# Kernel tuning notes

Measured on AMD Instinct MI355X. Metric: run time of the kernel, lower is better.

The kernel has to match this reference:

```python
import jax, jax.numpy as jnp
import numpy as np

D_MODEL = 1024
NUM_HEADS = 16
HEAD_DIM = D_MODEL // NUM_HEADS


def setup_inputs() -> dict:
    key = jax.random.key(0)
    k_x, k_qkv, k_o = jax.random.split(key, 3)
    B, L = 2, 2048
    x = jax.random.normal(k_x, (B, L, D_MODEL), dtype=jnp.float32)
    # torch Linear weight [out, in]; y = x @ W.T. Scale ~ kaiming-uniform-ish.
    s = 1.0 / np.sqrt(D_MODEL)
    W_qkv = jax.random.uniform(k_qkv, (3 * D_MODEL, D_MODEL), dtype=jnp.float32, minval=-s, maxval=s)
    W_o = jax.random.uniform(k_o, (D_MODEL, D_MODEL), dtype=jnp.float32, minval=-s, maxval=s)
    return {"x": x, "W_qkv": W_qkv, "W_o": W_o}


def reference(x, W_qkv, W_o):
    B, L, D = x.shape
    H, dk = NUM_HEADS, HEAD_DIM
    qkv = (x @ W_qkv.T).reshape(B, L, 3, H, dk)
    q = qkv[:, :, 0].transpose(0, 2, 1, 3)  # [B,H,L,dk]
    k = qkv[:, :, 1].transpose(0, 2, 1, 3)
    v = qkv[:, :, 2].transpose(0, 2, 1, 3)
    scale = 1.0 / np.sqrt(dk).astype(np.float32)
    attn = jnp.einsum('bhqd,bhkd->bhqk', q, k) * scale  # [B,H,L,L]
    causal = jnp.tril(jnp.ones((L, L), dtype=bool))
    attn = jnp.where(causal, attn, -jnp.inf)
    attn = jax.nn.softmax(attn, axis=-1)
    y = jnp.einsum('bhqk,bhkd->bhqd', attn, v)  # [B,H,L,dk]
    y = y.transpose(0, 2, 1, 3).reshape(B, L, D)
    return y @ W_o.T
```

## Files before the change

kernel.cpp:

```cpp
#include <hip/hip_runtime.h>

typedef unsigned short u16;
typedef unsigned int   u32;

typedef __attribute__((ext_vector_type(4))) float  f32x4;
typedef __attribute__((ext_vector_type(8))) __bf16 bf16x8;

#define B_  2
#define L_  2048
#define H_  16

__device__ static inline u16 f2bf(float f) {
  u32 u = __builtin_bit_cast(u32, f);
  u32 r = u + 0x7fffu + ((u >> 16) & 1u);
  return (u16)(r >> 16);
}
__device__ static inline u32 pack2(float a, float b) {
  return (u32)f2bf(a) | ((u32)f2bf(b) << 16);
}
__device__ static inline u32 pack2t(float a, float b) {
  return __builtin_amdgcn_perm(__builtin_bit_cast(u32, b),
                               __builtin_bit_cast(u32, a), 0x07060302u);
}

__device__ static inline void gload_lds16(const u16* g, u16* lds) {
  __builtin_amdgcn_global_load_lds((__attribute__((address_space(1))) void*)(g),
                                   (__attribute__((address_space(3))) void*)(lds),
                                   16, 0, 0);
}

__global__ __launch_bounds__(256) void cvt3_kernel(
    const float4* __restrict__ a, uint2* __restrict__ ao, int na,
    const float4* __restrict__ b, uint2* __restrict__ bo, int nb,
    const float4* __restrict__ c, uint2* __restrict__ co, int nc)
{
  const int step = gridDim.x * 256;
  constexpr int nq = 1024 * 1024 / 4;
  for (int i = blockIdx.x * 256 + threadIdx.x; i < na; i += step) {
    float4 f = a[i];
    ao[i] = make_uint2(pack2(f.x, f.y), pack2(f.z, f.w));
  }
  for (int i = blockIdx.x * 256 + threadIdx.x; i < nb; i += step) {
    float4 f = b[i];
    const float s = (i < nq) ? 0.125f : 1.0f;
    bo[i] = make_uint2(pack2(f.x * s, f.y * s), pack2(f.z * s, f.w * s));
  }
  for (int i = blockIdx.x * 256 + threadIdx.x; i < nc; i += step) {
    float4 f = c[i];
    co[i] = make_uint2(pack2(f.x, f.y), pack2(f.z, f.w));
  }
}

template <bool OUT_F32, int NT, bool DBUF>
__global__ __launch_bounds__(256) void gemm_bt_kernel(
    const u16* __restrict__ A, const u16* __restrict__ Bt, void* __restrict__ Cv,
    const int K, const int N)
{
  constexpr int NB = DBUF ? 2 : 1;
  constexpr int JT = NT / 32;
  __shared__ __attribute__((aligned(16))) u16 Al[NB][128 * 64];
  __shared__ __attribute__((aligned(16))) u16 Bl[NB][NT * 64];

  const int tid  = threadIdx.x;
  const int w    = tid >> 6;
  const int lane = tid & 63;
  const int m0 = blockIdx.y * 128;
  const int n0 = blockIdx.x * NT;
  const int mo = (w >> 1) * 64;
  const int no = (w & 1) * (NT / 2);

  const int sr8  = lane >> 3;
  const int scol = (((lane & 7) ^ ((lane >> 3) & 7)) * 8);

  const f32x4 zero = {0.f, 0.f, 0.f, 0.f};
  f32x4 acc[4][JT];
  #pragma unroll
  for (int i = 0; i < 4; ++i)
    #pragma unroll
    for (int j = 0; j < JT; ++j) acc[i][j] = zero;

  const int frow = lane & 15;
  const int fg   = lane >> 4;

  auto stage = [&](int buf, int k0) {
    #pragma unroll
    for (int inst = 0; inst < 4; ++inst) {
      const int r = w * 32 + inst * 8 + sr8;
      gload_lds16(A + (size_t)(m0 + r) * K + k0 + scol, &Al[buf][(w * 32 + inst * 8) * 64]);
    }
    #pragma unroll
    for (int inst = 0; inst < NT / 32; ++inst) {
      const int r = w * (NT / 4) + inst * 8 + sr8;
      gload_lds16(Bt + (size_t)(n0 + r) * K + k0 + scol, &Bl[buf][(w * (NT / 4) + inst * 8) * 64]);
    }
  };

  if (DBUF) stage(0, 0);

  int cur = 0;
  for (int k0 = 0; k0 < K; k0 += 64) {
    __syncthreads();
    if (DBUF) {
      if (k0 + 64 < K) stage(cur ^ 1, k0 + 64);
    } else {
      stage(0, k0);
      __syncthreads();
    }
    #pragma unroll
    for (int ks = 0; ks < 2; ++ks) {
      const int fco = ((ks * 4 + fg) ^ (frow & 7)) * 8;
      bf16x8 af[4], bfr[JT];
      #pragma unroll
      for (int i = 0; i < 4; ++i)
        af[i] = *(const bf16x8*)&Al[cur][(mo + i * 16 + frow) * 64 + fco];
      #pragma unroll
      for (int j = 0; j < JT; ++j)
        bfr[j] = *(const bf16x8*)&Bl[cur][(no + j * 16 + frow) * 64 + fco];
      #pragma unroll
      for (int i = 0; i < 4; ++i)
        #pragma unroll
        for (int j = 0; j < JT; ++j)
          acc[i][j] = __builtin_amdgcn_mfma_f32_16x16x32_bf16(af[i], bfr[j], acc[i][j], 0, 0, 0);
    }
    if (DBUF) cur ^= 1;
  }

  const int crow0 = m0 + mo + (lane >> 4) * 4;
  const int ccol0 = n0 + no + (lane & 15);
  #pragma unroll
  for (int i = 0; i < 4; ++i)
    #pragma unroll
    for (int j = 0; j < JT; ++j)
      #pragma unroll
      for (int r = 0; r < 4; ++r) {
        const size_t idx = (size_t)(crow0 + i * 16 + r) * N + (ccol0 + j * 16);
        if (OUT_F32) ((float*)Cv)[idx] = acc[i][j][r];
        else         ((u16*)Cv)[idx]   = f2bf(acc[i][j][r]);
      }
}

__global__ __launch_bounds__(256) void attn_mfma_kernel(const u16* __restrict__ qkv,
                                                        u16* __restrict__ y)
{
  __shared__ __attribute__((aligned(16))) unsigned char smem[40960];

  const int tid  = threadIdx.x;
  const int w    = tid >> 6;
  const int lane = tid & 63;
  const int fr   = lane & 15;
  const int fg   = lane >> 4;
  const int bh   = blockIdx.x;
  const int bb   = bh >> 4;
  const int hh   = bh & 15;
  const size_t rb = (size_t)bb * L_;

  const int a  = blockIdx.y & 7;
  const int cc = blockIdx.y >> 3;
  const int qt = (cc == 0) ? a : (cc == 1) ? (31 - a) : (cc == 2) ? (8 + a) : (23 - a);

  u16* Kt  = (u16*)(smem);
  u32* Vtd = (u32*)(smem + 16384);
  u32* PTd = (u32*)(smem + 32768) + w * 512;

  const int kkp = lane & 31;
  const int dc  = 2 * w + (lane >> 5);

  const int ksr = w * 16 + (lane >> 3);
  const int ksc = (((lane & 7) ^ ((lane >> 3) & 7)) * 8);
  const int kco0 = ((fg) ^ (fr & 7)) * 8;
  const int kco1 = ((4 + fg) ^ (fr & 7)) * 8;

  const int cro0 = 4 * ((fg) ^ (fr & 7));
  const int cro1 = 4 * ((4 + fg) ^ (fr & 7));
  const int pwo  = 4 * (fr & 7);

  const f32x4 zero = {0.f, 0.f, 0.f, 0.f};

  const int q0 = qt * 64;
  const int qw = q0 + w * 16;
  const int n  = qt + 1;

  const bf16x8 qf0 = *(const bf16x8*)(qkv + (rb + qw + fr) * 3072 + hh * 64 + fg * 8);
  const bf16x8 qf1 = *(const bf16x8*)(qkv + (rb + qw + fr) * 3072 + hh * 64 + 32 + fg * 8);

  f32x4 oacc[4];
  #pragma unroll
  for (int mt = 0; mt < 4; ++mt) oacc[mt] = zero;
  float lsum = 0.f;

  {
    #pragma unroll
    for (int inst = 0; inst < 2; ++inst)
      gload_lds16(qkv + (rb + ksr + inst * 8) * 3072 + 1024 + hh * 64 + ksc,
                  &Kt[(w * 16 + inst * 8) * 64]);
    const u16* vp = qkv + (rb + 2 * kkp) * 3072 + 2048 + hh * 64 + dc * 8;
    uint4 va = *(const uint4*)vp;
    uint4 vb = *(const uint4*)(vp + 3072);
    u16 a16[8], b16[8];
    *(uint4*)a16 = va; *(uint4*)b16 = vb;
    #pragma unroll
    for (int i = 0; i < 8; ++i)
      Vtd[(dc * 8 + i) * 32 + 4 * ((kkp >> 2) ^ i) + (kkp & 3)] =
          (u32)a16[i] | ((u32)b16[i] << 16);
  }

  int cur = 0;
  for (int it = 0; it < n; ++it) {
    __syncthreads();

    const int  kt       = it * 64;
    const bool havenext = (it + 1) < n;
    uint4 va, vb;
    if (havenext) {
      #pragma unroll
      for (int inst = 0; inst < 2; ++inst)
        gload_lds16(qkv + (rb + kt + 64 + ksr + inst * 8) * 3072 + 1024 + hh * 64 + ksc,
                    &Kt[(cur ^ 1) * 4096 + (w * 16 + inst * 8) * 64]);
      const u16* vp = qkv + (rb + kt + 64 + 2 * kkp) * 3072 + 2048 + hh * 64 + dc * 8;
      va = *(const uint4*)vp;
      vb = *(const uint4*)(vp + 3072);
    }

    f32x4 sacc[4];
    #pragma unroll
    for (int nt = 0; nt < 4; ++nt) sacc[nt] = zero;
    __builtin_amdgcn_s_setprio(1);
    #pragma unroll
    for (int nt = 0; nt < 4; ++nt) {
      bf16x8 kf0 = *(const bf16x8*)&Kt[cur * 4096 + (nt * 16 + fr) * 64 + kco0];
      sacc[nt] = __builtin_amdgcn_mfma_f32_16x16x32_bf16(kf0, qf0, sacc[nt], 0, 0, 0);
      bf16x8 kf1 = *(const bf16x8*)&Kt[cur * 4096 + (nt * 16 + fr) * 64 + kco1];
      sacc[nt] = __builtin_amdgcn_mfma_f32_16x16x32_bf16(kf1, qf1, sacc[nt], 0, 0, 0);
    }
    __builtin_amdgcn_s_setprio(0);

    if (kt == q0) {
      #pragma unroll
      for (int nt = 0; nt < 4; ++nt) {
        float p[4];
        #pragma unroll
        for (int r = 0; r < 4; ++r) {
          p[r] = (nt * 16 + 4 * fg + r > w * 16 + fr) ? 0.f : __expf(sacc[nt][r]);
          lsum += p[r];
        }
        *(uint2*)&PTd[fr * 32 + ((8 * nt + 2 * fg) ^ pwo)] =
            make_uint2(pack2t(p[0], p[1]), pack2t(p[2], p[3]));
      }
    } else {
      #pragma unroll
      for (int nt = 0; nt < 4; ++nt) {
        float p[4];
        #pragma unroll
        for (int r = 0; r < 4; ++r) {
          p[r] = __expf(sacc[nt][r]);
          lsum += p[r];
        }
        *(uint2*)&PTd[fr * 32 + ((8 * nt + 2 * fg) ^ pwo)] =
            make_uint2(pack2t(p[0], p[1]), pack2t(p[2], p[3]));
      }
    }

    __builtin_amdgcn_s_setprio(1);
    #pragma unroll
    for (int ks = 0; ks < 2; ++ks) {
      bf16x8 pf = *(const bf16x8*)&PTd[fr * 32 + (ks ? cro1 : cro0)];
      #pragma unroll
      for (int mt = 0; mt < 4; ++mt) {
        bf16x8 vf = *(const bf16x8*)&Vtd[cur * 2048 + (mt * 16 + fr) * 32 + (ks ? cro1 : cro0)];
        oacc[mt] = __builtin_amdgcn_mfma_f32_16x16x32_bf16(vf, pf, oacc[mt], 0, 0, 0);
      }
    }
    __builtin_amdgcn_s_setprio(0);

    if (havenext) {
      u16 a16[8], b16[8];
      *(uint4*)a16 = va; *(uint4*)b16 = vb;
      #pragma unroll
      for (int i = 0; i < 8; ++i)
        Vtd[(cur ^ 1) * 2048 + (dc * 8 + i) * 32 + 4 * ((kkp >> 2) ^ i) + (kkp & 3)] =
            (u32)a16[i] | ((u32)b16[i] << 16);
    }
    cur ^= 1;
  }

  lsum += __shfl_xor(lsum, 16);
  lsum += __shfl_xor(lsum, 32);
  const float inv = 1.f / lsum;

  u16* yp = y + (rb + qw + fr) * 1024 + hh * 64 + 4 * fg;
  #pragma unroll
  for (int mt = 0; mt < 4; ++mt) {
    f32x4 o = oacc[mt];
    *(uint2*)(yp + mt * 16) = make_uint2(pack2(o[0] * inv, o[1] * inv),
                                         pack2(o[2] * inv, o[3] * inv));
  }
}

extern "C" void kernel_launch(void* const* d_in, const int* in_sizes, int n_in,
                              void* d_out, int out_size, void* d_ws, size_t ws_size,
                              hipStream_t stream)
{
  const float* x    = (const float*)d_in[0];
  const float* Wqkv = (const float*)d_in[1];
  const float* Wo   = (const float*)d_in[2];
  float* out = (float*)d_out;

  u16* xb    = (u16*)d_ws;
  u16* Wqkvb = xb    + (size_t)4096 * 1024;
  u16* Wob   = Wqkvb + (size_t)3072 * 1024;
  u16* qkv   = Wob   + (size_t)1024 * 1024;
  u16* y     = qkv   + (size_t)4096 * 3072;

  cvt3_kernel<<<dim3(2048), dim3(256), 0, stream>>>(
      (const float4*)x,    (uint2*)xb,    4096 * 1024 / 4,
      (const float4*)Wqkv, (uint2*)Wqkvb, 3072 * 1024 / 4,
      (const float4*)Wo,   (uint2*)Wob,   1024 * 1024 / 4);

  gemm_bt_kernel<false, 128, false><<<dim3(3072 / 128, 4096 / 128), dim3(256), 0, stream>>>(
      xb, Wqkvb, qkv, 1024, 3072);
  attn_mfma_kernel<<<dim3(B_ * H_, 32), dim3(256), 0, stream>>>(qkv, y);
  gemm_bt_kernel<true, 64, true><<<dim3(1024 / 64, 4096 / 128), dim3(256), 0, stream>>>(
      y, Wob, out, 1024, 1024);
}
```

Before: 169.3 us.

## Use two waves per attention block with 32 query rows each and register-permuted P

The attention kernel now runs 128 threads per block, and each wave handles 32 query rows instead of 16, so every K and V fragment read from LDS feeds two MFMAs. The P tile no longer goes through an LDS round trip. It is rearranged in registers with permlane32/permlane16 swaps, which removes the PTd buffer and shrinks LDS to 32 KB. Each thread now stages more K and V per iteration. The change raises register pressure and halves the threads per block, which may reduce latency hiding.

```diff
diff --git a/kernel.cpp b/kernel.cpp
--- a/kernel.cpp
+++ b/kernel.cpp
@@ -4,6 +4,7 @@
 typedef unsigned int   u32;
 
 typedef __attribute__((ext_vector_type(4))) float  f32x4;
+typedef __attribute__((ext_vector_type(4))) u32    u32x4;
 typedef __attribute__((ext_vector_type(8))) __bf16 bf16x8;
 
 #define B_  2
@@ -21,6 +22,15 @@
 __device__ static inline u32 pack2t(float a, float b) {
   return __builtin_amdgcn_perm(__builtin_bit_cast(u32, b),
                                __builtin_bit_cast(u32, a), 0x07060302u);
+}
+
+__device__ static inline void swap32p(u32& a, u32& b) {
+  auto r = __builtin_amdgcn_permlane32_swap(a, b, false, false);
+  a = r[0]; b = r[1];
+}
+__device__ static inline void swap16p(u32& a, u32& b) {
+  auto r = __builtin_amdgcn_permlane16_swap(a, b, false, false);
+  a = r[0]; b = r[1];
 }
 
 __device__ static inline void gload_lds16(const u16* g, u16* lds) {
@@ -139,10 +149,10 @@
       }
 }
 
-__global__ __launch_bounds__(256) void attn_mfma_kernel(const u16* __restrict__ qkv,
+__global__ __launch_bounds__(128) void attn_mfma_kernel(const u16* __restrict__ qkv,
                                                         u16* __restrict__ y)
 {
-  __shared__ __attribute__((aligned(16))) unsigned char smem[40960];
+  __shared__ __attribute__((aligned(16))) unsigned char smem[32768];
 
   const int tid  = threadIdx.x;
   const int w    = tid >> 6;
@@ -160,48 +170,65 @@
 
   u16* Kt  = (u16*)(smem);
   u32* Vtd = (u32*)(smem + 16384);
-  u32* PTd = (u32*)(smem + 32768) + w * 512;
-
-  const int kkp = lane & 31;
-  const int dc  = 2 * w + (lane >> 5);
-
-  const int ksr = w * 16 + (lane >> 3);
-  const int ksc = (((lane & 7) ^ ((lane >> 3) & 7)) * 8);
+
+  const int kkp = tid & 31;
+  const int dc  = tid >> 5;
+
+  const int ksr  = lane >> 3;
+  const int ksc  = (((lane & 7) ^ ((lane >> 3) & 7)) * 8);
   const int kco0 = ((fg) ^ (fr & 7)) * 8;
   const int kco1 = ((4 + fg) ^ (fr & 7)) * 8;
-
   const int cro0 = 4 * ((fg) ^ (fr & 7));
   const int cro1 = 4 * ((4 + fg) ^ (fr & 7));
-  const int pwo  = 4 * (fr & 7);
+
+  const int q0 = qt * 64;
+  const int qw = q0 + w * 32;
+  const int n  = qt + 1;
+
+  const bf16x8 qf00 = *(const bf16x8*)(qkv + (rb + qw + fr) * 3072 + hh * 64 + fg * 8);
+  const bf16x8 qf01 = *(const bf16x8*)(qkv + (rb + qw + fr) * 3072 + hh * 64 + 32 + fg * 8);
+  const bf16x8 qf10 = *(const bf16x8*)(qkv + (rb + qw + 16 + fr) * 3072 + hh * 64 + fg * 8);
+  const bf16x8 qf11 = *(const bf16x8*)(qkv + (rb + qw + 16 + fr) * 3072 + hh * 64 + 32 + fg * 8);
 
   const f32x4 zero = {0.f, 0.f, 0.f, 0.f};
-
-  const int q0 = qt * 64;
-  const int qw = q0 + w * 16;
-  const int n  = qt + 1;
-
-  const bf16x8 qf0 = *(const bf16x8*)(qkv + (rb + qw + fr) * 3072 + hh * 64 + fg * 8);
-  const bf16x8 qf1 = *(const bf16x8*)(qkv + (rb + qw + fr) * 3072 + hh * 64 + 32 + fg * 8);
-
-  f32x4 oacc[4];
+  f32x4 oacc[4][2];
   #pragma unroll
-  for (int mt = 0; mt < 4; ++mt) oacc[mt] = zero;
-  float lsum = 0.f;
+  for (int mt = 0; mt < 4; ++mt) {
+    oacc[mt][0] = zero;
+    oacc[mt][1] = zero;
+  }
+  float ls0 = 0.f, ls1 = 0.f;
+
+  auto stageK = [&](int buf, int kt) {
+    #pragma unroll
+    for (int i = 0; i < 4; ++i)
+      gload_lds16(qkv + (rb + kt + w * 32 + i * 8 + ksr) * 3072 + 1024 + hh * 64 + ksc,
+                  &Kt[buf * 4096 + (w * 32 + i * 8) * 64]);
+  };
+  auto loadV = [&](int kt, uint4* va) {
+    const u16* vp = qkv + (rb + kt + 2 * kkp) * 3072 + 2048 + hh * 64 + dc * 16;
+    va[0] = *(const uint4*)(vp);
+    va[1] = *(const uint4*)(vp + 8);
+    va[2] = *(const uint4*)(vp + 3072);
+    va[3] = *(const uint4*)(vp + 3072 + 8);
+  };
+  auto writeV = [&](int buf, const uint4* va) {
+    u16 a16[16], b16[16];
+    *(uint4*)(a16)     = va[0]; *(uint4*)(a16 + 8) = va[1];
+    *(uint4*)(b16)     = va[2]; *(uint4*)(b16 + 8) = va[3];
+    #pragma unroll
+    for (int i = 0; i < 16; ++i) {
+      const int d = dc * 16 + i;
+      Vtd[buf * 2048 + d * 32 + 4 * ((kkp >> 2) ^ (i & 7)) + (kkp & 3)] =
+          (u32)a16[i] | ((u32)b16[i] << 16);
+    }
+  };
 
   {
-    #pragma unroll
-    for (int inst = 0; inst < 2; ++inst)
-      gload_lds16(qkv + (rb + ksr + inst * 8) * 3072 + 1024 + hh * 64 + ksc,
-                  &Kt[(w * 16 + inst * 8) * 64]);
-    const u16* vp = qkv + (rb + 2 * kkp) * 3072 + 2048 + hh * 64 + dc * 8;
-    uint4 va = *(const uint4*)vp;
-    uint4 vb = *(const uint4*)(vp + 3072);
-    u16 a16[8], b16[8];
-    *(uint4*)a16 = va; *(uint4*)b16 = vb;
-    #pragma unroll
-    for (int i = 0; i < 8; ++i)
-      Vtd[(dc * 8 + i) * 32 + 4 * ((kkp >> 2) ^ i) + (kkp & 3)] =
-          (u32)a16[i] | ((u32)b16[i] << 16);
+    stageK(0, 0);
+    uint4 va[4];
+    loadV(0, va);
+    writeV(0, va);
   }
 
   int cur = 0;
@@ -210,89 +237,104 @@
 
     const int  kt       = it * 64;
     const bool havenext = (it + 1) < n;
-    uint4 va, vb;
+    uint4 va[4];
     if (havenext) {
-      #pragma unroll
-      for (int inst = 0; inst < 2; ++inst)
-        gload_lds16(qkv + (rb + kt + 64 + ksr + inst * 8) * 3072 + 1024 + hh * 64 + ksc,
-                    &Kt[(cur ^ 1) * 4096 + (w * 16 + inst * 8) * 64]);
-      const u16* vp = qkv + (rb + kt + 64 + 2 * kkp) * 3072 + 2048 + hh * 64 + dc * 8;
-      va = *(const uint4*)vp;
-      vb = *(const uint4*)(vp + 3072);
-    }
-
-    f32x4 sacc[4];
-    #pragma unroll
-    for (int nt = 0; nt < 4; ++nt) sacc[nt] = zero;
+      stageK(cur ^ 1, kt + 64);
+      loadV(kt + 64, va);
+    }
+
+    f32x4 sacc[4][2];
+    #pragma unroll
+    for (int nt = 0; nt < 4; ++nt) { sacc[nt][0] = zero; sacc[nt][1] = zero; }
     __builtin_amdgcn_s_setprio(1);
     #pragma unroll
     for (int nt = 0; nt < 4; ++nt) {
       bf16x8 kf0 = *(const bf16x8*)&Kt[cur * 4096 + (nt * 16 + fr) * 64 + kco0];
-      sacc[nt] = __builtin_amdgcn_mfma_f32_16x16x32_bf16(kf0, qf0, sacc[nt], 0, 0, 0);
       bf16x8 kf1 = *(const bf16x8*)&Kt[cur * 4096 + (nt * 16 + fr) * 64 + kco1];
-      sacc[nt] = __builtin_amdgcn_mfma_f32_16x16x32_bf16(kf1, qf1, sacc[nt], 0, 0, 0);
+      sacc[nt][0] = __builtin_amdgcn_mfma_f32_16x16x32_bf16(kf0, qf00, sacc[nt][0], 0, 0, 0);
+      sacc[nt][0] = __builtin_amdgcn_mfma_f32_16x16x32_bf16(kf1, qf01, sacc[nt][0], 0, 0, 0);
+      sacc[nt][1] = __builtin_amdgcn_mfma_f32_16x16x32_bf16(kf0, qf10, sacc[nt][1], 0, 0, 0);
+      sacc[nt][1] = __builtin_amdgcn_mfma_f32_16x16x32_bf16(kf1, qf11, sacc[nt][1], 0, 0, 0);
     }
     __builtin_amdgcn_s_setprio(0);
 
+    u32 pk[4][2][2];
     if (kt == q0) {
       #pragma unroll
-      for (int nt = 0; nt < 4; ++nt) {
-        float p[4];
+      for (int nt = 0; nt < 4; ++nt)
         #pragma unroll
-        for (int r = 0; r < 4; ++r) {
-          p[r] = (nt * 16 + 4 * fg + r > w * 16 + fr) ? 0.f : __expf(sacc[nt][r]);
-          lsum += p[r];
+        for (int qc = 0; qc < 2; ++qc) {
+          float p[4];
+          #pragma unroll
+          for (int r = 0; r < 4; ++r) {
+            p[r] = (nt * 16 + 4 * fg + r > w * 32 + qc * 16 + fr)
+                       ? 0.f : __expf(sacc[nt][qc][r]);
+            if (qc == 0) ls0 += p[r]; else ls1 += p[r];
+          }
+          pk[nt][qc][0] = pack2t(p[0], p[1]);
+          pk[nt][qc][1] = pack2t(p[2], p[3]);
         }
-        *(uint2*)&PTd[fr * 32 + ((8 * nt + 2 * fg) ^ pwo)] =
-            make_uint2(pack2t(p[0], p[1]), pack2t(p[2], p[3]));
+    } else {
+      #pragma unroll
+      for (int nt = 0; nt < 4; ++nt)
+        #pragma unroll
+        for (int qc = 0; qc < 2; ++qc) {
+          float p[4];
+          #pragma unroll
+          for (int r = 0; r < 4; ++r) {
+            p[r] = __expf(sacc[nt][qc][r]);
+            if (qc == 0) ls0 += p[r]; else ls1 += p[r];
+          }
+          pk[nt][qc][0] = pack2t(p[0], p[1]);
+          pk[nt][qc][1] = pack2t(p[2], p[3]);
+        }
+    }
+
+    __builtin_amdgcn_s_setprio(1);
+    #pragma unroll
+    for (int ks = 0; ks < 2; ++ks) {
+      bf16x8 pf[2];
+      #pragma unroll
+      for (int qc = 0; qc < 2; ++qc) {
+        u32 P0 = pk[2 * ks][qc][0], Q0 = pk[2 * ks + 1][qc][0];
+        u32 P1 = pk[2 * ks][qc][1], Q1 = pk[2 * ks + 1][qc][1];
+        swap32p(P0, Q0);
+        swap32p(P1, Q1);
+        swap16p(P0, Q0);
+        swap16p(P1, Q1);
+        pf[qc] = __builtin_bit_cast(bf16x8, (u32x4){P0, P1, Q0, Q1});
       }
-    } else {
-      #pragma unroll
-      for (int nt = 0; nt < 4; ++nt) {
-        float p[4];
-        #pragma unroll
-        for (int r = 0; r < 4; ++r) {
-          p[r] = __expf(sacc[nt][r]);
-          lsum += p[r];
-        }
-        *(uint2*)&PTd[fr * 32 + ((8 * nt + 2 * fg) ^ pwo)] =
-            make_uint2(pack2t(p[0], p[1]), pack2t(p[2], p[3]));
+      const int cro = ks ? cro1 : cro0;
+      #pragma unroll
+      for (int mt = 0; mt < 4; ++mt) {
+        bf16x8 vf = *(const bf16x8*)&Vtd[cur * 2048 + (mt * 16 + fr) * 32 + cro];
+        oacc[mt][0] = __builtin_amdgcn_mfma_f32_16x16x32_bf16(vf, pf[0], oacc[mt][0], 0, 0, 0);
+        oacc[mt][1] = __builtin_amdgcn_mfma_f32_16x16x32_bf16(vf, pf[1], oacc[mt][1], 0, 0, 0);
       }
     }
-
-    __builtin_amdgcn_s_setprio(1);
-    #pragma unroll
-    for (int ks = 0; ks < 2; ++ks) {
-      bf16x8 pf = *(const bf16x8*)&PTd[fr * 32 + (ks ? cro1 : cro0)];
-      #pragma unroll
-      for (int mt = 0; mt < 4; ++mt) {
-        bf16x8 vf = *(const bf16x8*)&Vtd[cur * 2048 + (mt * 16 + fr) * 32 + (ks ? cro1 : cro0)];
-        oacc[mt] = __builtin_amdgcn_mfma_f32_16x16x32_bf16(vf, pf, oacc[mt], 0, 0, 0);
-      }
-    }
     __builtin_amdgcn_s_setprio(0);
 
-    if (havenext) {
-      u16 a16[8], b16[8];
-      *(uint4*)a16 = va; *(uint4*)b16 = vb;
-      #pragma unroll
-      for (int i = 0; i < 8; ++i)
-        Vtd[(cur ^ 1) * 2048 + (dc * 8 + i) * 32 + 4 * ((kkp >> 2) ^ i) + (kkp & 3)] =
-            (u32)a16[i] | ((u32)b16[i] << 16);
-    }
+    if (havenext) writeV(cur ^ 1, va);
     cur ^= 1;
   }
 
-  lsum += __shfl_xor(lsum, 16);
-  lsum += __shfl_xor(lsum, 32);
-  const float inv = 1.f / lsum;
-
-  u16* yp = y + (rb + qw + fr) * 1024 + hh * 64 + 4 * fg;
+  ls0 += __shfl_xor(ls0, 16);
+  ls0 += __shfl_xor(ls0, 32);
+  ls1 += __shfl_xor(ls1, 16);
+  ls1 += __shfl_xor(ls1, 32);
+  const float inv0 = 1.f / ls0;
+  const float inv1 = 1.f / ls1;
+
+  u16* yp0 = y + (rb + qw + fr) * 1024 + hh * 64 + 4 * fg;
+  u16* yp1 = y + (rb + qw + 16 + fr) * 1024 + hh * 64 + 4 * fg;
   #pragma unroll
   for (int mt = 0; mt < 4; ++mt) {
-    f32x4 o = oacc[mt];
-    *(uint2*)(yp + mt * 16) = make_uint2(pack2(o[0] * inv, o[1] * inv),
-                                         pack2(o[2] * inv, o[3] * inv));
+    f32x4 o0 = oacc[mt][0];
+    f32x4 o1 = oacc[mt][1];
+    *(uint2*)(yp0 + mt * 16) = make_uint2(pack2(o0[0] * inv0, o0[1] * inv0),
+                                          pack2(o0[2] * inv0, o0[3] * inv0));
+    *(uint2*)(yp1 + mt * 16) = make_uint2(pack2(o1[0] * inv1, o1[1] * inv1),
+                                          pack2(o1[2] * inv1, o1[3] * inv1));
   }
 }
 
@@ -318,7 +360,7 @@
 
   gemm_bt_kernel<false, 128, false><<<dim3(3072 / 128, 4096 / 128), dim3(256), 0, stream>>>(
       xb, Wqkvb, qkv, 1024, 3072);
-  attn_mfma_kernel<<<dim3(B_ * H_, 32), dim3(256), 0, stream>>>(qkv, y);
+  attn_mfma_kernel<<<dim3(B_ * H_, 32), dim3(128), 0, stream>>>(qkv, y);
   gemm_bt_kernel<true, 64, true><<<dim3(1024 / 64, 4096 / 128), dim3(256), 0, stream>>>(
       y, Wob, out, 1024, 1024);
 }
```

New measurement: 172.4 us. About the same (+1.8%).

## Use 32x32 MFMA with register-resident P and split-K waves in attention

Applied to the files above, without the earlier changes.

Rewrites the attention kernel to use 32x32x16 bf16 MFMA tiles. Each wave now owns a 32-query by 32-key quadrant, and the P matrix stays in registers, rearranged with permlane32_swap, so the LDS P buffer is gone. The two key-half waves combine partial outputs and row sums through LDS at the end, and fully masked diagonal quadrants are skipped. LDS use drops and a 4-blocks-per-CU launch bound is added. In exchange the kernel needs an extra reduction step, and the larger accumulators raise register pressure.

```diff
diff --git a/kernel.cpp b/kernel.cpp
--- a/kernel.cpp
+++ b/kernel.cpp
@@ -3,8 +3,10 @@
 typedef unsigned short u16;
 typedef unsigned int   u32;
 
-typedef __attribute__((ext_vector_type(4))) float  f32x4;
-typedef __attribute__((ext_vector_type(8))) __bf16 bf16x8;
+typedef __attribute__((ext_vector_type(4)))  float  f32x4;
+typedef __attribute__((ext_vector_type(16))) float  f32x16;
+typedef __attribute__((ext_vector_type(4)))  u32    u32x4;
+typedef __attribute__((ext_vector_type(8)))  __bf16 bf16x8;
 
 #define B_  2
 #define L_  2048
@@ -21,6 +23,11 @@
 __device__ static inline u32 pack2t(float a, float b) {
   return __builtin_amdgcn_perm(__builtin_bit_cast(u32, b),
                                __builtin_bit_cast(u32, a), 0x07060302u);
+}
+
+__device__ static inline void swap32p(u32& a, u32& b) {
+  auto r = __builtin_amdgcn_permlane32_swap(a, b, false, false);
+  a = r[0]; b = r[1];
 }
 
 __device__ static inline void gload_lds16(const u16* g, u16* lds) {
@@ -139,16 +146,18 @@
       }
 }
 
-__global__ __launch_bounds__(256) void attn_mfma_kernel(const u16* __restrict__ qkv,
-                                                        u16* __restrict__ y)
+__global__ __launch_bounds__(256, 4) void attn_mfma_kernel(const u16* __restrict__ qkv,
+                                                           u16* __restrict__ y)
 {
-  __shared__ __attribute__((aligned(16))) unsigned char smem[40960];
+  __shared__ __attribute__((aligned(16))) unsigned char smem[32768];
 
   const int tid  = threadIdx.x;
   const int w    = tid >> 6;
   const int lane = tid & 63;
-  const int fr   = lane & 15;
-  const int fg   = lane >> 4;
+  const int ql   = lane & 31;
+  const int hi   = lane >> 5;
+  const int qh   = w >> 1;
+  const int kh   = w & 1;
   const int bh   = blockIdx.x;
   const int bb   = bh >> 4;
   const int hh   = bh & 15;
@@ -158,50 +167,54 @@
   const int cc = blockIdx.y >> 3;
   const int qt = (cc == 0) ? a : (cc == 1) ? (31 - a) : (cc == 2) ? (8 + a) : (23 - a);
 
-  u16* Kt  = (u16*)(smem);
-  u32* Vtd = (u32*)(smem + 16384);
-  u32* PTd = (u32*)(smem + 32768) + w * 512;
+  u16* Kt   = (u16*)(smem);
+  u32* Vtd  = (u32*)(smem + 16384);
+  float* Ocmb = (float*)smem;
+  float* Lcmb = (float*)(smem + 16384);
 
   const int kkp = lane & 31;
   const int dc  = 2 * w + (lane >> 5);
 
   const int ksr = w * 16 + (lane >> 3);
   const int ksc = (((lane & 7) ^ ((lane >> 3) & 7)) * 8);
-  const int kco0 = ((fg) ^ (fr & 7)) * 8;
-  const int kco1 = ((4 + fg) ^ (fr & 7)) * 8;
-
-  const int cro0 = 4 * ((fg) ^ (fr & 7));
-  const int cro1 = 4 * ((4 + fg) ^ (fr & 7));
-  const int pwo  = 4 * (fr & 7);
-
-  const f32x4 zero = {0.f, 0.f, 0.f, 0.f};
 
   const int q0 = qt * 64;
-  const int qw = q0 + w * 16;
+  const int qb = q0 + qh * 32;
   const int n  = qt + 1;
 
-  const bf16x8 qf0 = *(const bf16x8*)(qkv + (rb + qw + fr) * 3072 + hh * 64 + fg * 8);
-  const bf16x8 qf1 = *(const bf16x8*)(qkv + (rb + qw + fr) * 3072 + hh * 64 + 32 + fg * 8);
-
-  f32x4 oacc[4];
+  bf16x8 qf[4];
   #pragma unroll
-  for (int mt = 0; mt < 4; ++mt) oacc[mt] = zero;
+  for (int s = 0; s < 4; ++s)
+    qf[s] = *(const bf16x8*)(qkv + (rb + qb + ql) * 3072 + hh * 64 + s * 16 + 8 * hi);
+
+  f32x16 oacc0 = {}, oacc1 = {};
   float lsum = 0.f;
 
-  {
+  auto stageK = [&](int buf, int kt) {
     #pragma unroll
     for (int inst = 0; inst < 2; ++inst)
-      gload_lds16(qkv + (rb + ksr + inst * 8) * 3072 + 1024 + hh * 64 + ksc,
-                  &Kt[(w * 16 + inst * 8) * 64]);
-    const u16* vp = qkv + (rb + 2 * kkp) * 3072 + 2048 + hh * 64 + dc * 8;
-    uint4 va = *(const uint4*)vp;
-    uint4 vb = *(const uint4*)(vp + 3072);
+      gload_lds16(qkv + (rb + kt + ksr + inst * 8) * 3072 + 1024 + hh * 64 + ksc,
+                  &Kt[buf * 4096 + (w * 16 + inst * 8) * 64]);
+  };
+  auto loadV = [&](int kt, uint4& va, uint4& vb) {
+    const u16* vp = qkv + (rb + kt + 2 * kkp) * 3072 + 2048 + hh * 64 + dc * 8;
+    va = *(const uint4*)vp;
+    vb = *(const uint4*)(vp + 3072);
+  };
+  auto writeV = [&](int buf, uint4 va, uint4 vb) {
     u16 a16[8], b16[8];
     *(uint4*)a16 = va; *(uint4*)b16 = vb;
     #pragma unroll
     for (int i = 0; i < 8; ++i)
-      Vtd[(dc * 8 + i) * 32 + 4 * ((kkp >> 2) ^ i) + (kkp & 3)] =
+      Vtd[buf * 2048 + (dc * 8 + i) * 32 + 4 * ((kkp >> 2) ^ i) + (kkp & 3)] =
           (u32)a16[i] | ((u32)b16[i] << 16);
+  };
+
+  {
+    stageK(0, 0);
+    uint4 va, vb;
+    loadV(0, va, vb);
+    writeV(0, va, vb);
   }
 
   int cur = 0;
@@ -212,87 +225,95 @@
     const bool havenext = (it + 1) < n;
     uint4 va, vb;
     if (havenext) {
-      #pragma unroll
-      for (int inst = 0; inst < 2; ++inst)
-        gload_lds16(qkv + (rb + kt + 64 + ksr + inst * 8) * 3072 + 1024 + hh * 64 + ksc,
-                    &Kt[(cur ^ 1) * 4096 + (w * 16 + inst * 8) * 64]);
-      const u16* vp = qkv + (rb + kt + 64 + 2 * kkp) * 3072 + 2048 + hh * 64 + dc * 8;
-      va = *(const uint4*)vp;
-      vb = *(const uint4*)(vp + 3072);
-    }
-
-    f32x4 sacc[4];
-    #pragma unroll
-    for (int nt = 0; nt < 4; ++nt) sacc[nt] = zero;
-    __builtin_amdgcn_s_setprio(1);
-    #pragma unroll
-    for (int nt = 0; nt < 4; ++nt) {
-      bf16x8 kf0 = *(const bf16x8*)&Kt[cur * 4096 + (nt * 16 + fr) * 64 + kco0];
-      sacc[nt] = __builtin_amdgcn_mfma_f32_16x16x32_bf16(kf0, qf0, sacc[nt], 0, 0, 0);
-      bf16x8 kf1 = *(const bf16x8*)&Kt[cur * 4096 + (nt * 16 + fr) * 64 + kco1];
-      sacc[nt] = __builtin_amdgcn_mfma_f32_16x16x32_bf16(kf1, qf1, sacc[nt], 0, 0, 0);
-    }
-    __builtin_amdgcn_s_setprio(0);
-
-    if (kt == q0) {
-      #pragma unroll
-      for (int nt = 0; nt < 4; ++nt) {
-        float p[4];
+      stageK(cur ^ 1, kt + 64);
+      loadV(kt + 64, va, vb);
+    }
+
+    const bool diag = (kt == q0);
+    if (!(diag && kh > qh)) {
+      f32x16 sacc = {};
+      __builtin_amdgcn_s_setprio(1);
+      #pragma unroll
+      for (int s = 0; s < 4; ++s) {
+        bf16x8 kf = *(const bf16x8*)&Kt[cur * 4096 + (kh * 32 + ql) * 64 +
+                                        (((2 * s + hi) ^ (ql & 7)) * 8)];
+        sacc = __builtin_amdgcn_mfma_f32_32x32x16_bf16(kf, qf[s], sacc, 0, 0, 0);
+      }
+      __builtin_amdgcn_s_setprio(0);
+
+      u32 u[8];
+      if (diag && kh == qh) {
         #pragma unroll
-        for (int r = 0; r < 4; ++r) {
-          p[r] = (nt * 16 + 4 * fg + r > w * 16 + fr) ? 0.f : __expf(sacc[nt][r]);
-          lsum += p[r];
+        for (int j = 0; j < 8; ++j) {
+          const int r0  = 2 * j;
+          const int k0r = (r0 & 3) + 8 * (r0 >> 2) + 4 * hi;
+          const float p0 = (k0r     > ql) ? 0.f : __expf(sacc[r0]);
+          const float p1 = (k0r + 1 > ql) ? 0.f : __expf(sacc[r0 + 1]);
+          lsum += p0 + p1;
+          u[j] = pack2t(p0, p1);
         }
-        *(uint2*)&PTd[fr * 32 + ((8 * nt + 2 * fg) ^ pwo)] =
-            make_uint2(pack2t(p[0], p[1]), pack2t(p[2], p[3]));
-      }
-    } else {
-      #pragma unroll
-      for (int nt = 0; nt < 4; ++nt) {
-        float p[4];
+      } else {
         #pragma unroll
-        for (int r = 0; r < 4; ++r) {
-          p[r] = __expf(sacc[nt][r]);
-          lsum += p[r];
+        for (int j = 0; j < 8; ++j) {
+          const float p0 = __expf(sacc[2 * j]);
+          const float p1 = __expf(sacc[2 * j + 1]);
+          lsum += p0 + p1;
+          u[j] = pack2t(p0, p1);
         }
-        *(uint2*)&PTd[fr * 32 + ((8 * nt + 2 * fg) ^ pwo)] =
-            make_uint2(pack2t(p[0], p[1]), pack2t(p[2], p[3]));
-      }
-    }
-
-    __builtin_amdgcn_s_setprio(1);
-    #pragma unroll
-    for (int ks = 0; ks < 2; ++ks) {
-      bf16x8 pf = *(const bf16x8*)&PTd[fr * 32 + (ks ? cro1 : cro0)];
-      #pragma unroll
-      for (int mt = 0; mt < 4; ++mt) {
-        bf16x8 vf = *(const bf16x8*)&Vtd[cur * 2048 + (mt * 16 + fr) * 32 + (ks ? cro1 : cro0)];
-        oacc[mt] = __builtin_amdgcn_mfma_f32_16x16x32_bf16(vf, pf, oacc[mt], 0, 0, 0);
-      }
-    }
-    __builtin_amdgcn_s_setprio(0);
-
-    if (havenext) {
-      u16 a16[8], b16[8];
-      *(uint4*)a16 = va; *(uint4*)b16 = vb;
-      #pragma unroll
-      for (int i = 0; i < 8; ++i)
-        Vtd[(cur ^ 1) * 2048 + (dc * 8 + i) * 32 + 4 * ((kkp >> 2) ^ i) + (kkp & 3)] =
-            (u32)a16[i] | ((u32)b16[i] << 16);
-    }
+      }
+
+      swap32p(u[0], u[2]); swap32p(u[1], u[3]);
+      swap32p(u[4], u[6]); swap32p(u[5], u[7]);
+      const bf16x8 pf0 = __builtin_bit_cast(bf16x8, (u32x4){u[0], u[1], u[2], u[3]});
+      const bf16x8 pf1 = __builtin_bit_cast(bf16x8, (u32x4){u[4], u[5], u[6], u[7]});
+
+      __builtin_amdgcn_s_setprio(1);
+      #pragma unroll
+      for (int dt = 0; dt < 2; ++dt) {
+        f32x16& oa = dt ? oacc1 : oacc0;
+        const int d = dt * 32 + ql;
+        bf16x8 vf0 = *(const bf16x8*)&Vtd[cur * 2048 + d * 32 + 4 * ((4 * kh + hi) ^ (ql & 7))];
+        oa = __builtin_amdgcn_mfma_f32_32x32x16_bf16(vf0, pf0, oa, 0, 0, 0);
+        bf16x8 vf1 = *(const bf16x8*)&Vtd[cur * 2048 + d * 32 + 4 * ((4 * kh + 2 + hi) ^ (ql & 7))];
+        oa = __builtin_amdgcn_mfma_f32_32x32x16_bf16(vf1, pf1, oa, 0, 0, 0);
+      }
+      __builtin_amdgcn_s_setprio(0);
+    }
+
+    if (havenext) writeV(cur ^ 1, va, vb);
     cur ^= 1;
   }
 
-  lsum += __shfl_xor(lsum, 16);
   lsum += __shfl_xor(lsum, 32);
-  const float inv = 1.f / lsum;
-
-  u16* yp = y + (rb + qw + fr) * 1024 + hh * 64 + 4 * fg;
-  #pragma unroll
-  for (int mt = 0; mt < 4; ++mt) {
-    f32x4 o = oacc[mt];
-    *(uint2*)(yp + mt * 16) = make_uint2(pack2(o[0] * inv, o[1] * inv),
-                                         pack2(o[2] * inv, o[3] * inv));
+
+  __syncthreads();
+  if (kh == 1) {
+    #pragma unroll
+    for (int dt = 0; dt < 2; ++dt)
+      #pragma unroll
+      for (int rq = 0; rq < 4; ++rq) {
+        const f32x16& oa = dt ? oacc1 : oacc0;
+        *(f32x4*)&Ocmb[(qh * 8 + dt * 4 + rq) * 256 + lane * 4] =
+            (f32x4){oa[4 * rq], oa[4 * rq + 1], oa[4 * rq + 2], oa[4 * rq + 3]};
+      }
+    if (hi == 0) Lcmb[qh * 32 + ql] = lsum;
+  }
+  __syncthreads();
+  if (kh == 0) {
+    const float inv = 1.f / (lsum + Lcmb[qh * 32 + ql]);
+    u16* yp = y + (rb + qb + ql) * 1024 + hh * 64;
+    #pragma unroll
+    for (int dt = 0; dt < 2; ++dt)
+      #pragma unroll
+      for (int rq = 0; rq < 4; ++rq) {
+        const f32x16& oa = dt ? oacc1 : oacc0;
+        const f32x4 oc = *(const f32x4*)&Ocmb[(qh * 8 + dt * 4 + rq) * 256 + lane * 4];
+        const float v0 = (oa[4 * rq]     + oc[0]) * inv;
+        const float v1 = (oa[4 * rq + 1] + oc[1]) * inv;
+        const float v2 = (oa[4 * rq + 2] + oc[2]) * inv;
+        const float v3 = (oa[4 * rq + 3] + oc[3]) * inv;
+        *(uint2*)(yp + dt * 32 + 8 * rq + 4 * hi) = make_uint2(pack2(v0, v1), pack2(v2, v3));
+      }
   }
 }
 
```

Result: faster. 159.2 us (-6.0%).
